# Kernel tuning notes

Hardware: AMD Instinct MI355X
Metric: run time of the kernel (lower is better)

The kernel has to match this reference:

```python
import jax, jax.numpy as jnp
import numpy as np

NUM_HEADS = 16
NUM_UNITS = 1024
NEG = -2.0**32 + 1.0
EPS = 1e-8


def setup_inputs() -> dict:
    key = jax.random.key(0)
    ks = jax.random.split(key, 8)
    B, T, C = 2, 2048, 1024
    U = NUM_UNITS
    x = jax.random.normal(ks[0], (B, T, C), dtype=jnp.float32)
    s = 1.0 / np.sqrt(C)
    Wq = jax.random.normal(ks[1], (C, U), dtype=jnp.float32) * s
    Wk = jax.random.normal(ks[2], (C, U), dtype=jnp.float32) * s
    Wv = jax.random.normal(ks[3], (C, U), dtype=jnp.float32) * s
    bq = jnp.zeros((U,), dtype=jnp.float32)
    bk = jnp.zeros((U,), dtype=jnp.float32)
    bv = jnp.zeros((U,), dtype=jnp.float32)
    gamma = jnp.ones((U,), dtype=jnp.float32)
    beta = jnp.zeros((U,), dtype=jnp.float32)
    return {"x": x, "Wq": Wq, "bq": bq, "Wk": Wk, "bk": bk,
            "Wv": Wv, "bv": bv, "gamma": gamma, "beta": beta}


def _attention(x, Wq, bq, Wk, bk, Wv, bv, gamma, beta):
    B, T, C = x.shape
    H = NUM_HEADS
    U = NUM_UNITS
    dh = U // H
    # Dense projections with relu activation (Keras Dense(activation='relu'))
    Q = jax.nn.relu(x @ Wq + bq)  # [B, T, U]
    K = jax.nn.relu(x @ Wk + bk)
    V = jax.nn.relu(x @ Wv + bv)
    # split into heads: tf.split(axis=2) + concat(axis=0) == [B, T, H, dh]
    Qh = Q.reshape(B, T, H, dh)
    Kh = K.reshape(B, T, H, dh)
    Vh = V.reshape(B, T, H, dh)
    # scaled dot-product scores: scale by sqrt(d_head) (K_ last dim after split)
    scores = jnp.einsum('bqhd,bkhd->bhqk', Qh, Kh) / np.sqrt(dh)
    # key mask: sign(|sum(keys, -1)|) over the ORIGINAL keys input (= x)
    key_mask = jnp.sign(jnp.abs(jnp.sum(x, axis=-1)))  # [B, Tk]
    scores = jnp.where(key_mask[:, None, None, :] == 0, NEG, scores)
    # causal mask (lower-triangular)
    tril = jnp.tril(jnp.ones((T, T), dtype=scores.dtype))
    scores = jnp.where(tril[None, None, :, :] == 0, NEG, scores)
    attn = jax.nn.softmax(scores, axis=-1)
    # query mask: multiply attention rows for zero queries
    query_mask = jnp.sign(jnp.abs(jnp.sum(x, axis=-1)))  # [B, Tq]
    attn = attn * query_mask[:, None, :, None]
    # dropout rate is 0 -> identity
    out = jnp.einsum('bhqk,bkhd->bqhd', attn, Vh).reshape(B, T, U)
    # residual with original queries
    out = out + x
    # layer norm over last axis (tf.nn.moments: biased variance)
    mean = jnp.mean(out, axis=-1, keepdims=True)
    var = jnp.mean((out - mean) ** 2, axis=-1, keepdims=True)
    normalized = (out - mean) / jnp.sqrt(var + EPS)
    return gamma * normalized + beta


def reference(x, Wq, bq, Wk, bk, Wv, bv, gamma, beta):
    return _attention(x, Wq, bq, Wk, bk, Wv, bv, gamma, beta)
```

## Files before the change

### kernel.cpp

```cpp
#include <hip/hip_runtime.h>
#include <math.h>

#define BB 2
#define TT 2048
#define CC 1024
#define UU 1024
#define HH 16
#define DH 64
#define BT (BB*TT)

typedef __attribute__((ext_vector_type(8))) __bf16 bf16x8;
typedef __attribute__((ext_vector_type(4))) __bf16 bf16x4;
typedef __attribute__((ext_vector_type(4))) float f32x4;

#define GLL16(g, l) __builtin_amdgcn_global_load_lds( \
    (__attribute__((address_space(1))) const void*)(g), \
    (__attribute__((address_space(3))) void*)(l), 16, 0, 0)

#define C2EXP 0.18033688011112042f
#define MBIAS 64.0f

__global__ __launch_bounds__(256) void prep_kernel(
    const float* __restrict__ x, float* __restrict__ kadd, __bf16* __restrict__ xb,
    const float* __restrict__ Wq, const float* __restrict__ Wk,
    const float* __restrict__ Wv, __bf16* __restrict__ Wt) {
    const int bx = blockIdx.x;
    const int t = threadIdx.x;
    if (bx < BT) {
        int row = bx;
        float4 v = *(const float4*)&x[(size_t)row * CC + t * 4];
        bf16x4 o;
        o[0] = (__bf16)v.x; o[1] = (__bf16)v.y; o[2] = (__bf16)v.z; o[3] = (__bf16)v.w;
        *(bf16x4*)&xb[(size_t)row * CC + t * 4] = o;
        float s = v.x + v.y + v.z + v.w;
#pragma unroll
        for (int off = 32; off; off >>= 1) s += __shfl_down(s, off, 64);
        __shared__ float red[4];
        int lane = t & 63, w = t >> 6;
        if (lane == 0) red[w] = s;
        __syncthreads();
        if (t == 0) {
            float tot = red[0] + red[1] + red[2] + red[3];
            kadd[row] = (tot == 0.f ? -1.0e30f : 0.f) - MBIAS;
        }
    } else {
        int bz = bx - BT;
        int z = bz >> 8, rem = bz & 255;
        const float* W = z == 0 ? Wq : (z == 1 ? Wk : Wv);
        __bf16* Out = Wt + (size_t)z * CC * UU;
        __shared__ float tile[64][65];
        int n0 = (rem & 15) * 64, k0 = (rem >> 4) * 64;
        int r = t >> 4, c4 = (t & 15) * 4;
#pragma unroll
        for (int i = 0; i < 4; ++i) {
            float4 v = *(const float4*)&W[(size_t)(k0 + r + i * 16) * UU + n0 + c4];
            tile[r + i * 16][c4 + 0] = v.x; tile[r + i * 16][c4 + 1] = v.y;
            tile[r + i * 16][c4 + 2] = v.z; tile[r + i * 16][c4 + 3] = v.w;
        }
        __syncthreads();
#pragma unroll
        for (int i = 0; i < 4; ++i) {
            int nr = r + i * 16;
            bf16x4 o;
            o[0] = (__bf16)tile[c4 + 0][nr]; o[1] = (__bf16)tile[c4 + 1][nr];
            o[2] = (__bf16)tile[c4 + 2][nr]; o[3] = (__bf16)tile[c4 + 3][nr];
            *(bf16x4*)&Out[(size_t)(n0 + nr) * CC + k0 + c4] = o;
        }
    }
}

__global__ __launch_bounds__(256, 4) void qkv_mfma(
    const __bf16* __restrict__ xb, const __bf16* __restrict__ Wt_all,
    const float* __restrict__ bq, const float* __restrict__ bk,
    const float* __restrict__ bv,
    __bf16* __restrict__ Qo, __bf16* __restrict__ Ko, __bf16* __restrict__ VTo) {
    const int z = blockIdx.z;
    const __bf16* Wt = Wt_all + (size_t)z * CC * UU;
    const float* bias = z == 0 ? bq : (z == 1 ? bk : bv);

    const int n0 = blockIdx.x * 128, m0 = blockIdx.y * 128;
    const int t = threadIdx.x, w = t >> 6, lane = t & 63;
    const int quad = lane >> 4, nn = lane & 15;
    const int wr = w >> 1, wc = w & 1;

    __shared__ __bf16 smem[2 * 128 * 64];
    __bf16* As = smem;
    __bf16* Bs = smem + 128 * 64;

    f32x4 acc[4][4];
#pragma unroll
    for (int i = 0; i < 4; ++i)
#pragma unroll
        for (int j = 0; j < 4; ++j) acc[i][j] = (f32x4){0.f, 0.f, 0.f, 0.f};

    for (int k0 = 0; k0 < CC; k0 += 64) {
        __syncthreads();
#pragma unroll
        for (int i = 0; i < 4; ++i) {
            int c = i * 256 + t;
            int row = c >> 3;
            int gc = ((c & 7) ^ (row & 7)) * 8;
            GLL16(&xb[(size_t)(m0 + row) * CC + k0 + gc], &As[c * 8]);
            GLL16(&Wt[(size_t)(n0 + row) * CC + k0 + gc], &Bs[c * 8]);
        }
        __syncthreads();
#pragma unroll
        for (int kk = 0; kk < 2; ++kk) {
            bf16x8 af[4], bfr[4];
#pragma unroll
            for (int i = 0; i < 4; ++i) {
                int R = wr * 64 + i * 16 + nn;
                af[i] = *(const bf16x8*)&As[R * 64 + (((kk * 4 + quad) ^ (R & 7)) * 8)];
            }
#pragma unroll
            for (int j = 0; j < 4; ++j) {
                int R = wc * 64 + j * 16 + nn;
                bfr[j] = *(const bf16x8*)&Bs[R * 64 + (((kk * 4 + quad) ^ (R & 7)) * 8)];
            }
#pragma unroll
            for (int i = 0; i < 4; ++i)
#pragma unroll
                for (int j = 0; j < 4; ++j)
                    acc[i][j] = __builtin_amdgcn_mfma_f32_16x16x32_bf16(af[i], bfr[j], acc[i][j], 0, 0, 0);
        }
    }

    __bf16* cw = &smem[w * 1024];
    float bv4[4];
#pragma unroll
    for (int j = 0; j < 4; ++j) bv4[j] = bias[n0 + wc * 64 + j * 16 + nn];

    if (z < 2) {
        __bf16* Out = z == 0 ? Qo : Ko;
#pragma unroll
        for (int i = 0; i < 4; ++i) {
            __syncthreads();
#pragma unroll
            for (int j = 0; j < 4; ++j)
#pragma unroll
                for (int r = 0; r < 4; ++r)
                    cw[(quad * 4 + r) * 64 + j * 16 + nn] =
                        (__bf16)fmaxf(acc[i][j][r] + bv4[j], 0.f);
            __syncthreads();
            int rr = lane >> 2, cc = (lane & 3) * 16;
            bf16x8 v0 = *(const bf16x8*)&cw[rr * 64 + cc];
            bf16x8 v1 = *(const bf16x8*)&cw[rr * 64 + cc + 8];
            size_t o = (size_t)(m0 + wr * 64 + i * 16 + rr) * UU + n0 + wc * 64 + cc;
            *(bf16x8*)&Out[o] = v0;
            *(bf16x8*)&Out[o + 8] = v1;
        }
    } else {
#pragma unroll
        for (int i = 0; i < 4; ++i) {
            __syncthreads();
#pragma unroll
            for (int j = 0; j < 4; ++j)
#pragma unroll
                for (int r = 0; r < 4; ++r)
                    cw[(j * 16 + nn) * 16 + quad * 4 + r] =
                        (__bf16)fmaxf(acc[i][j][r] + bv4[j], 0.f);
            __syncthreads();
            bf16x8 v0 = *(const bf16x8*)&cw[lane * 16];
            bf16x8 v1 = *(const bf16x8*)&cw[lane * 16 + 8];
            size_t o = (size_t)(n0 + wc * 64 + lane) * BT + m0 + wr * 64 + i * 16;
            *(bf16x8*)&VTo[o] = v0;
            *(bf16x8*)&VTo[o + 8] = v1;
        }
    }
}

__global__ __launch_bounds__(256, 4) void attn_mfma(
    const __bf16* __restrict__ Q, const __bf16* __restrict__ K,
    const __bf16* __restrict__ Vt, const float* __restrict__ kadd,
    __bf16* __restrict__ Ob) {
    const int bx = blockIdx.x;
    const int bh = blockIdx.y, b = bh >> 4, h = bh & 15;
    const int j = bh >> 3;
    const int xj = (j & 2) ? ((bx + 16) & 31) : bx;
    const int qt = (j & 1) ? (31 - xj) : xj;
    const int col0 = h * 64, rowbase = b * TT, q0 = qt * 64;

    const int t = threadIdx.x;
    const int w = t >> 6, lane = t & 63, quad = lane >> 4, nn = lane & 15;
    const int s7 = nn & 7;

    __shared__ __align__(16) __bf16 ks[2][64 * 64];
    __shared__ __align__(16) __bf16 vt[2][64 * 64];
    __shared__ __align__(16) __bf16 ps[64 * 64];

    const int c0 = t, c1 = 256 + t;
    const int r0 = c0 >> 3, g0 = ((c0 & 7) ^ (r0 & 7)) * 8;
    const int r1 = c1 >> 3, g1 = ((c1 & 7) ^ (r1 & 7)) * 8;

    GLL16(&Q[(size_t)(rowbase + q0 + r0) * UU + col0 + g0], &ps[c0 * 8]);
    GLL16(&Q[(size_t)(rowbase + q0 + r1) * UU + col0 + g1], &ps[c1 * 8]);
    GLL16(&K[(size_t)(rowbase + r0) * UU + col0 + g0], &ks[0][c0 * 8]);
    GLL16(&K[(size_t)(rowbase + r1) * UU + col0 + g1], &ks[0][c1 * 8]);
    GLL16(&Vt[(size_t)(col0 + r0) * BT + rowbase + g0], &vt[0][c0 * 8]);
    GLL16(&Vt[(size_t)(col0 + r1) * BT + rowbase + g1], &vt[0][c1 * 8]);
    __syncthreads();

    const int prow = 16 * w + nn;
    bf16x8 bq0 = *(const bf16x8*)&ps[prow * 64 + ((quad ^ (prow & 7)) * 8)];
    bf16x8 bq1 = *(const bf16x8*)&ps[prow * 64 + (((4 + quad) ^ (prow & 7)) * 8)];

    float lp = 0.f;
    f32x4 oc[4];
#pragma unroll
    for (int dt = 0; dt < 4; ++dt) oc[dt] = (f32x4){0.f, 0.f, 0.f, 0.f};
    const int qg = q0 + 16 * w + nn;

    for (int kt = 0; kt <= qt; ++kt) {
        const int cur = kt & 1;
        const int k0 = kt * 64;
        f32x4 ka[4];
#pragma unroll
        for (int ct = 0; ct < 4; ++ct)
            ka[ct] = *(const f32x4*)&kadd[rowbase + k0 + ct * 16 + quad * 4];
        if (kt < qt) {
            const int kn = k0 + 64;
            GLL16(&K[(size_t)(rowbase + kn + r0) * UU + col0 + g0], &ks[cur ^ 1][c0 * 8]);
            GLL16(&K[(size_t)(rowbase + kn + r1) * UU + col0 + g1], &ks[cur ^ 1][c1 * 8]);
            GLL16(&Vt[(size_t)(col0 + r0) * BT + rowbase + kn + g0], &vt[cur ^ 1][c0 * 8]);
            GLL16(&Vt[(size_t)(col0 + r1) * BT + rowbase + kn + g1], &vt[cur ^ 1][c1 * 8]);
        }

        const bool diag = (kt == qt);
        const __bf16* ksc = ks[cur];
        const __bf16* vtc = vt[cur];

#pragma unroll
        for (int ct = 0; ct < 4; ++ct) {
            int krow = ct * 16 + nn;
            bf16x8 a0 = *(const bf16x8*)&ksc[krow * 64 + ((quad ^ s7) * 8)];
            bf16x8 a1 = *(const bf16x8*)&ksc[krow * 64 + (((4 + quad) ^ s7) * 8)];
            f32x4 sc = (f32x4){0.f, 0.f, 0.f, 0.f};
            sc = __builtin_amdgcn_mfma_f32_16x16x32_bf16(a0, bq0, sc, 0, 0, 0);
            sc = __builtin_amdgcn_mfma_f32_16x16x32_bf16(a1, bq1, sc, 0, 0, 0);
            bf16x4 pw;
#pragma unroll
            for (int r = 0; r < 4; ++r) {
                int key = k0 + ct * 16 + quad * 4 + r;
                float arg = fmaf(sc[r], C2EXP, ka[ct][r]);
                if (diag && key > qg) arg = -1.0e30f;
                float p = exp2f(arg);
                lp += p;
                pw[r] = (__bf16)p;
            }
            int chunk = ct * 2 + (quad >> 1);
            *(bf16x4*)&ps[prow * 64 + ((chunk ^ (prow & 7)) * 8) + (quad & 1) * 4] = pw;
        }
        bf16x8 bp0 = *(const bf16x8*)&ps[prow * 64 + ((quad ^ (prow & 7)) * 8)];
        bf16x8 bp1 = *(const bf16x8*)&ps[prow * 64 + (((4 + quad) ^ (prow & 7)) * 8)];
#pragma unroll
        for (int dt = 0; dt < 4; ++dt) {
            int vrow = dt * 16 + nn;
            bf16x8 a0 = *(const bf16x8*)&vtc[vrow * 64 + ((quad ^ s7) * 8)];
            bf16x8 a1 = *(const bf16x8*)&vtc[vrow * 64 + (((4 + quad) ^ s7) * 8)];
            oc[dt] = __builtin_amdgcn_mfma_f32_16x16x32_bf16(a0, bp0, oc[dt], 0, 0, 0);
            oc[dt] = __builtin_amdgcn_mfma_f32_16x16x32_bf16(a1, bp1, oc[dt], 0, 0, 0);
        }
        __syncthreads();
    }

    float l = lp;
    l += __shfl_xor(l, 16, 64);
    l += __shfl_xor(l, 32, 64);
    int grow = rowbase + qg;
    float qsel = (kadd[grow] < -1.0e29f) ? 0.f : 1.f;
    float mult = qsel / fmaxf(l, 1e-37f);
#pragma unroll
    for (int dt = 0; dt < 4; ++dt) {
        bf16x4 ov;
        ov[0] = (__bf16)(oc[dt][0] * mult); ov[1] = (__bf16)(oc[dt][1] * mult);
        ov[2] = (__bf16)(oc[dt][2] * mult); ov[3] = (__bf16)(oc[dt][3] * mult);
        *(bf16x4*)&Ob[(size_t)grow * UU + col0 + dt * 16 + quad * 4] = ov;
    }
}

__global__ __launch_bounds__(256) void ln_kernel(
    const __bf16* __restrict__ Ob, const float* __restrict__ x,
    const float* __restrict__ gamma, const float* __restrict__ beta,
    float* __restrict__ out) {
    int row = blockIdx.x;
    size_t base = (size_t)row * UU;
    int t = threadIdx.x;
    bf16x4 ov = *(const bf16x4*)&Ob[base + t * 4];
    float4 xv = *(const float4*)&x[base + t * 4];
    float v0 = (float)ov[0] + xv.x, v1 = (float)ov[1] + xv.y;
    float v2 = (float)ov[2] + xv.z, v3 = (float)ov[3] + xv.w;
    float s1 = v0 + v1 + v2 + v3;
    float s2 = v0 * v0 + v1 * v1 + v2 * v2 + v3 * v3;
#pragma unroll
    for (int off = 32; off; off >>= 1) {
        s1 += __shfl_down(s1, off, 64);
        s2 += __shfl_down(s2, off, 64);
    }
    __shared__ float r1[4], r2[4];
    int lane = t & 63, w = t >> 6;
    if (lane == 0) { r1[w] = s1; r2[w] = s2; }
    __syncthreads();
    s1 = r1[0] + r1[1] + r1[2] + r1[3];
    s2 = r2[0] + r2[1] + r2[2] + r2[3];
    float mean = s1 * (1.0f / 1024.0f);
    float var = s2 * (1.0f / 1024.0f) - mean * mean;
    float rstd = rsqrtf(var + 1e-8f);
    float4 g = *(const float4*)&gamma[t * 4];
    float4 be = *(const float4*)&beta[t * 4];
    float4 ores;
    ores.x = g.x * (v0 - mean) * rstd + be.x;
    ores.y = g.y * (v1 - mean) * rstd + be.y;
    ores.z = g.z * (v2 - mean) * rstd + be.z;
    ores.w = g.w * (v3 - mean) * rstd + be.w;
    *(float4*)&out[base + t * 4] = ores;
}

extern "C" void kernel_launch(void* const* d_in, const int* in_sizes, int n_in,
                              void* d_out, int out_size, void* d_ws, size_t ws_size,
                              hipStream_t stream) {
    const float* x     = (const float*)d_in[0];
    const float* Wq    = (const float*)d_in[1];
    const float* bq    = (const float*)d_in[2];
    const float* Wk    = (const float*)d_in[3];
    const float* bk    = (const float*)d_in[4];
    const float* Wv    = (const float*)d_in[5];
    const float* bv    = (const float*)d_in[6];
    const float* gamma = (const float*)d_in[7];
    const float* beta  = (const float*)d_in[8];
    float* out = (float*)d_out;

    char* wsb = (char*)d_ws;
    const size_t MB = 1024ull * 1024;
    __bf16* xb = (__bf16*)(wsb);
    __bf16* Wt = (__bf16*)(wsb + 8 * MB);
    __bf16* Ob = (__bf16*)(wsb);
    __bf16* Qb = (__bf16*)(wsb + 16 * MB);
    __bf16* Kb = (__bf16*)(wsb + 24 * MB);
    __bf16* Vt = (__bf16*)(wsb + 32 * MB);
    float* kadd = (float*)(wsb + 40 * MB);

    prep_kernel<<<dim3(BT + 768), dim3(256), 0, stream>>>(x, kadd, xb, Wq, Wk, Wv, Wt);
    qkv_mfma<<<dim3(UU / 128, BT / 128, 3), dim3(256), 0, stream>>>(
        xb, Wt, bq, bk, bv, Qb, Kb, Vt);
    attn_mfma<<<dim3(32, BB * HH), dim3(256), 0, stream>>>(Qb, Kb, Vt, kadd, Ob);
    ln_kernel<<<dim3(BT), dim3(256), 0, stream>>>(Ob, x, gamma, beta, out);
}
```

Measured before the change: 173.8 us.

## Enlarge attention query tile to 128 rows with 512-thread blocks sharing K/V tiles

The attention kernel now handles 128 query rows per block with 8 waves instead of 64 rows with 4 waves, so each K/V tile loaded into shared memory is reused by twice as many query rows. This halves K/V global traffic per query and halves the block count. Waves covering the first 64 rows skip the last key tile, and the diagonal mask is computed per half. The costs are fewer blocks in flight, a simpler load-balancing remap, more shared memory per block, and idle waves on the final tile.

```diff
diff --git a/kernel.cpp b/kernel.cpp
--- a/kernel.cpp
+++ b/kernel.cpp
@@ -169,16 +169,15 @@
     }
 }
 
-__global__ __launch_bounds__(256, 4) void attn_mfma(
+__global__ __launch_bounds__(512, 4) void attn_mfma(
     const __bf16* __restrict__ Q, const __bf16* __restrict__ K,
     const __bf16* __restrict__ Vt, const float* __restrict__ kadd,
     __bf16* __restrict__ Ob) {
     const int bx = blockIdx.x;
     const int bh = blockIdx.y, b = bh >> 4, h = bh & 15;
     const int j = bh >> 3;
-    const int xj = (j & 2) ? ((bx + 16) & 31) : bx;
-    const int qt = (j & 1) ? (31 - xj) : xj;
-    const int col0 = h * 64, rowbase = b * TT, q0 = qt * 64;
+    const int qt = (j & 2) ? (15 - bx) : bx;
+    const int col0 = h * 64, rowbase = b * TT, q0 = qt * 128;
 
     const int t = threadIdx.x;
     const int w = t >> 6, lane = t & 63, quad = lane >> 4, nn = lane & 15;
@@ -186,79 +185,80 @@
 
     __shared__ __align__(16) __bf16 ks[2][64 * 64];
     __shared__ __align__(16) __bf16 vt[2][64 * 64];
-    __shared__ __align__(16) __bf16 ps[64 * 64];
-
-    const int c0 = t, c1 = 256 + t;
-    const int r0 = c0 >> 3, g0 = ((c0 & 7) ^ (r0 & 7)) * 8;
-    const int r1 = c1 >> 3, g1 = ((c1 & 7) ^ (r1 & 7)) * 8;
-
-    GLL16(&Q[(size_t)(rowbase + q0 + r0) * UU + col0 + g0], &ps[c0 * 8]);
+    __shared__ __align__(16) __bf16 ps[128 * 64];
+
+    const int r0 = t >> 3, g0 = ((t & 7) ^ (r0 & 7)) * 8;
+    const int c1 = 512 + t, r1 = c1 >> 3, g1 = ((c1 & 7) ^ (r1 & 7)) * 8;
+
+    GLL16(&Q[(size_t)(rowbase + q0 + r0) * UU + col0 + g0], &ps[t * 8]);
     GLL16(&Q[(size_t)(rowbase + q0 + r1) * UU + col0 + g1], &ps[c1 * 8]);
-    GLL16(&K[(size_t)(rowbase + r0) * UU + col0 + g0], &ks[0][c0 * 8]);
-    GLL16(&K[(size_t)(rowbase + r1) * UU + col0 + g1], &ks[0][c1 * 8]);
-    GLL16(&Vt[(size_t)(col0 + r0) * BT + rowbase + g0], &vt[0][c0 * 8]);
-    GLL16(&Vt[(size_t)(col0 + r1) * BT + rowbase + g1], &vt[0][c1 * 8]);
+    GLL16(&K[(size_t)(rowbase + r0) * UU + col0 + g0], &ks[0][t * 8]);
+    GLL16(&Vt[(size_t)(col0 + r0) * BT + rowbase + g0], &vt[0][t * 8]);
     __syncthreads();
 
-    const int prow = 16 * w + nn;
-    bf16x8 bq0 = *(const bf16x8*)&ps[prow * 64 + ((quad ^ (prow & 7)) * 8)];
-    bf16x8 bq1 = *(const bf16x8*)&ps[prow * 64 + (((4 + quad) ^ (prow & 7)) * 8)];
+    const int prow = (w & 3) * 16 + nn + ((w >> 2) << 6);
+    const int p7 = prow & 7;
+    bf16x8 bq0 = *(const bf16x8*)&ps[prow * 64 + ((quad ^ p7) * 8)];
+    bf16x8 bq1 = *(const bf16x8*)&ps[prow * 64 + (((4 + quad) ^ p7) * 8)];
 
     float lp = 0.f;
     f32x4 oc[4];
 #pragma unroll
     for (int dt = 0; dt < 4; ++dt) oc[dt] = (f32x4){0.f, 0.f, 0.f, 0.f};
-    const int qg = q0 + 16 * w + nn;
-
-    for (int kt = 0; kt <= qt; ++kt) {
+    const int lr = prow & 63;
+    const int qg = q0 + prow;
+    const int kend = 2 * qt + 1;
+
+    for (int kt = 0; kt <= kend; ++kt) {
         const int cur = kt & 1;
         const int k0 = kt * 64;
         f32x4 ka[4];
 #pragma unroll
         for (int ct = 0; ct < 4; ++ct)
             ka[ct] = *(const f32x4*)&kadd[rowbase + k0 + ct * 16 + quad * 4];
-        if (kt < qt) {
+        if (kt < kend) {
             const int kn = k0 + 64;
-            GLL16(&K[(size_t)(rowbase + kn + r0) * UU + col0 + g0], &ks[cur ^ 1][c0 * 8]);
-            GLL16(&K[(size_t)(rowbase + kn + r1) * UU + col0 + g1], &ks[cur ^ 1][c1 * 8]);
-            GLL16(&Vt[(size_t)(col0 + r0) * BT + rowbase + kn + g0], &vt[cur ^ 1][c0 * 8]);
-            GLL16(&Vt[(size_t)(col0 + r1) * BT + rowbase + kn + g1], &vt[cur ^ 1][c1 * 8]);
-        }
-
-        const bool diag = (kt == qt);
-        const __bf16* ksc = ks[cur];
-        const __bf16* vtc = vt[cur];
-
-#pragma unroll
-        for (int ct = 0; ct < 4; ++ct) {
-            int krow = ct * 16 + nn;
-            bf16x8 a0 = *(const bf16x8*)&ksc[krow * 64 + ((quad ^ s7) * 8)];
-            bf16x8 a1 = *(const bf16x8*)&ksc[krow * 64 + (((4 + quad) ^ s7) * 8)];
-            f32x4 sc = (f32x4){0.f, 0.f, 0.f, 0.f};
-            sc = __builtin_amdgcn_mfma_f32_16x16x32_bf16(a0, bq0, sc, 0, 0, 0);
-            sc = __builtin_amdgcn_mfma_f32_16x16x32_bf16(a1, bq1, sc, 0, 0, 0);
-            bf16x4 pw;
-#pragma unroll
-            for (int r = 0; r < 4; ++r) {
-                int key = k0 + ct * 16 + quad * 4 + r;
-                float arg = fmaf(sc[r], C2EXP, ka[ct][r]);
-                if (diag && key > qg) arg = -1.0e30f;
-                float p = exp2f(arg);
-                lp += p;
-                pw[r] = (__bf16)p;
+            GLL16(&K[(size_t)(rowbase + kn + r0) * UU + col0 + g0], &ks[cur ^ 1][t * 8]);
+            GLL16(&Vt[(size_t)(col0 + r0) * BT + rowbase + kn + g0], &vt[cur ^ 1][t * 8]);
+        }
+
+        const bool skip = (w < 4) && (kt == kend);
+        if (!skip) {
+            const bool diag = (kt == kend - 1 + (w >> 2));
+            const __bf16* ksc = ks[cur];
+            const __bf16* vtc = vt[cur];
+
+#pragma unroll
+            for (int ct = 0; ct < 4; ++ct) {
+                int krow = ct * 16 + nn;
+                bf16x8 a0 = *(const bf16x8*)&ksc[krow * 64 + ((quad ^ s7) * 8)];
+                bf16x8 a1 = *(const bf16x8*)&ksc[krow * 64 + (((4 + quad) ^ s7) * 8)];
+                f32x4 sc = (f32x4){0.f, 0.f, 0.f, 0.f};
+                sc = __builtin_amdgcn_mfma_f32_16x16x32_bf16(a0, bq0, sc, 0, 0, 0);
+                sc = __builtin_amdgcn_mfma_f32_16x16x32_bf16(a1, bq1, sc, 0, 0, 0);
+                bf16x4 pw;
+#pragma unroll
+                for (int r = 0; r < 4; ++r) {
+                    int kl = ct * 16 + quad * 4 + r;
+                    float arg = fmaf(sc[r], C2EXP, ka[ct][r]);
+                    if (diag && kl > lr) arg = -1.0e30f;
+                    float p = exp2f(arg);
+                    lp += p;
+                    pw[r] = (__bf16)p;
+                }
+                int chunk = ct * 2 + (quad >> 1);
+                *(bf16x4*)&ps[prow * 64 + ((chunk ^ p7) * 8) + (quad & 1) * 4] = pw;
             }
-            int chunk = ct * 2 + (quad >> 1);
-            *(bf16x4*)&ps[prow * 64 + ((chunk ^ (prow & 7)) * 8) + (quad & 1) * 4] = pw;
-        }
-        bf16x8 bp0 = *(const bf16x8*)&ps[prow * 64 + ((quad ^ (prow & 7)) * 8)];
-        bf16x8 bp1 = *(const bf16x8*)&ps[prow * 64 + (((4 + quad) ^ (prow & 7)) * 8)];
-#pragma unroll
-        for (int dt = 0; dt < 4; ++dt) {
-            int vrow = dt * 16 + nn;
-            bf16x8 a0 = *(const bf16x8*)&vtc[vrow * 64 + ((quad ^ s7) * 8)];
-            bf16x8 a1 = *(const bf16x8*)&vtc[vrow * 64 + (((4 + quad) ^ s7) * 8)];
-            oc[dt] = __builtin_amdgcn_mfma_f32_16x16x32_bf16(a0, bp0, oc[dt], 0, 0, 0);
-            oc[dt] = __builtin_amdgcn_mfma_f32_16x16x32_bf16(a1, bp1, oc[dt], 0, 0, 0);
+            bf16x8 bp0 = *(const bf16x8*)&ps[prow * 64 + ((quad ^ p7) * 8)];
+            bf16x8 bp1 = *(const bf16x8*)&ps[prow * 64 + (((4 + quad) ^ p7) * 8)];
+#pragma unroll
+            for (int dt = 0; dt < 4; ++dt) {
+                int vrow = dt * 16 + nn;
+                bf16x8 a0 = *(const bf16x8*)&vtc[vrow * 64 + ((quad ^ s7) * 8)];
+                bf16x8 a1 = *(const bf16x8*)&vtc[vrow * 64 + (((4 + quad) ^ s7) * 8)];
+                oc[dt] = __builtin_amdgcn_mfma_f32_16x16x32_bf16(a0, bp0, oc[dt], 0, 0, 0);
+                oc[dt] = __builtin_amdgcn_mfma_f32_16x16x32_bf16(a1, bp1, oc[dt], 0, 0, 0);
+            }
         }
         __syncthreads();
     }
@@ -342,6 +342,6 @@
     prep_kernel<<<dim3(BT + 768), dim3(256), 0, stream>>>(x, kadd, xb, Wq, Wk, Wv, Wt);
     qkv_mfma<<<dim3(UU / 128, BT / 128, 3), dim3(256), 0, stream>>>(
         xb, Wt, bq, bk, bv, Qb, Kb, Vt);
-    attn_mfma<<<dim3(32, BB * HH), dim3(256), 0, stream>>>(Qb, Kb, Vt, kadd, Ob);
+    attn_mfma<<<dim3(16, BB * HH), dim3(512), 0, stream>>>(Qb, Kb, Vt, kadd, Ob);
     ln_kernel<<<dim3(BT), dim3(256), 0, stream>>>(Ob, x, gamma, beta, out);
 }
```

Result: slower. 181.7 us (+4.5%).

## Triple-buffer K tiles with explicit vmcnt waits in causal attention kernel

Applied to the files above, without the earlier changes.

Restructures the attention main loop so K is prefetched two tiles ahead in a triple buffer and V one tile ahead, synchronising with fine-grained s_waitcnt vmcnt plus s_barrier instead of a full __syncthreads. Q fragments now load straight from global memory into registers rather than staging through LDS, kadd values are prefetched one iteration ahead, and the diagonal tile is peeled so the main loop carries no mask check. The intent is to hide global load latency behind the MFMA work. The extra LDS buffer lowers the occupancy hint from 4 to 3 blocks per CU. Inline asm wait counts and reads from fixed ring offsets make correctness depend on the exact ordering of the loads.

```diff
diff --git a/kernel.cpp b/kernel.cpp
--- a/kernel.cpp
+++ b/kernel.cpp
@@ -169,7 +169,7 @@
     }
 }
 
-__global__ __launch_bounds__(256, 4) void attn_mfma(
+__global__ __launch_bounds__(256, 3) void attn_mfma(
     const __bf16* __restrict__ Q, const __bf16* __restrict__ K,
     const __bf16* __restrict__ Vt, const float* __restrict__ kadd,
     __bf16* __restrict__ Ob) {
@@ -184,84 +184,113 @@
     const int w = t >> 6, lane = t & 63, quad = lane >> 4, nn = lane & 15;
     const int s7 = nn & 7;
 
-    __shared__ __align__(16) __bf16 ks[2][64 * 64];
+    __shared__ __align__(16) __bf16 ks[3][64 * 64];
     __shared__ __align__(16) __bf16 vt[2][64 * 64];
     __shared__ __align__(16) __bf16 ps[64 * 64];
 
-    const int c0 = t, c1 = 256 + t;
+    const int c0 = t;
     const int r0 = c0 >> 3, g0 = ((c0 & 7) ^ (r0 & 7)) * 8;
-    const int r1 = c1 >> 3, g1 = ((c1 & 7) ^ (r1 & 7)) * 8;
-
-    GLL16(&Q[(size_t)(rowbase + q0 + r0) * UU + col0 + g0], &ps[c0 * 8]);
-    GLL16(&Q[(size_t)(rowbase + q0 + r1) * UU + col0 + g1], &ps[c1 * 8]);
-    GLL16(&K[(size_t)(rowbase + r0) * UU + col0 + g0], &ks[0][c0 * 8]);
-    GLL16(&K[(size_t)(rowbase + r1) * UU + col0 + g1], &ks[0][c1 * 8]);
-    GLL16(&Vt[(size_t)(col0 + r0) * BT + rowbase + g0], &vt[0][c0 * 8]);
-    GLL16(&Vt[(size_t)(col0 + r1) * BT + rowbase + g1], &vt[0][c1 * 8]);
-    __syncthreads();
-
     const int prow = 16 * w + nn;
-    bf16x8 bq0 = *(const bf16x8*)&ps[prow * 64 + ((quad ^ (prow & 7)) * 8)];
-    bf16x8 bq1 = *(const bf16x8*)&ps[prow * 64 + (((4 + quad) ^ (prow & 7)) * 8)];
+    const int qg = q0 + prow;
+
+    const __bf16* kp0 = &K[(size_t)(rowbase + r0) * UU + col0 + g0];
+    const __bf16* kp1 = kp0 + 32 * (size_t)UU;
+    const __bf16* vp0 = &Vt[(size_t)(col0 + r0) * BT + rowbase + g0];
+    const __bf16* vp1 = vp0 + 32 * (size_t)BT;
+    const float* kap = &kadd[rowbase + quad * 4];
+
+    f32x4 ka[4];
+#pragma unroll
+    for (int ct = 0; ct < 4; ++ct) ka[ct] = *(const f32x4*)&kap[ct * 16];
+    kap += 64;
+    const __bf16* qrow = &Q[(size_t)(rowbase + qg) * UU + col0];
+    bf16x8 bq0 = *(const bf16x8*)&qrow[quad * 8];
+    bf16x8 bq1 = *(const bf16x8*)&qrow[32 + quad * 8];
+    __builtin_amdgcn_sched_barrier(0);
+    GLL16(kp0, &ks[0][c0 * 8]);
+    GLL16(kp1, &ks[0][c0 * 8 + 2048]);
+    GLL16(vp0, &vt[0][c0 * 8]);
+    GLL16(vp1, &vt[0][c0 * 8 + 2048]);
+    kp0 += 64 * (size_t)UU; kp1 += 64 * (size_t)UU;
+    vp0 += 64; vp1 += 64;
+    __builtin_amdgcn_sched_barrier(0);
+    GLL16(kp0, &ks[0][4096 + c0 * 8]);
+    GLL16(kp1, &ks[0][4096 + c0 * 8 + 2048]);
+    kp0 += 64 * (size_t)UU; kp1 += 64 * (size_t)UU;
+    __builtin_amdgcn_sched_barrier(0);
+    asm volatile("s_waitcnt vmcnt(2)" ::: "memory");
+    __builtin_amdgcn_s_barrier();
 
     float lp = 0.f;
     f32x4 oc[4];
 #pragma unroll
     for (int dt = 0; dt < 4; ++dt) oc[dt] = (f32x4){0.f, 0.f, 0.f, 0.f};
-    const int qg = q0 + 16 * w + nn;
-
-    for (int kt = 0; kt <= qt; ++kt) {
-        const int cur = kt & 1;
-        const int k0 = kt * 64;
-        f32x4 ka[4];
-#pragma unroll
-        for (int ct = 0; ct < 4; ++ct)
-            ka[ct] = *(const f32x4*)&kadd[rowbase + k0 + ct * 16 + quad * 4];
-        if (kt < qt) {
-            const int kn = k0 + 64;
-            GLL16(&K[(size_t)(rowbase + kn + r0) * UU + col0 + g0], &ks[cur ^ 1][c0 * 8]);
-            GLL16(&K[(size_t)(rowbase + kn + r1) * UU + col0 + g1], &ks[cur ^ 1][c1 * 8]);
-            GLL16(&Vt[(size_t)(col0 + r0) * BT + rowbase + kn + g0], &vt[cur ^ 1][c0 * 8]);
-            GLL16(&Vt[(size_t)(col0 + r1) * BT + rowbase + kn + g1], &vt[cur ^ 1][c1 * 8]);
-        }
-
-        const bool diag = (kt == qt);
-        const __bf16* ksc = ks[cur];
-        const __bf16* vtc = vt[cur];
-
-#pragma unroll
-        for (int ct = 0; ct < 4; ++ct) {
-            int krow = ct * 16 + nn;
-            bf16x8 a0 = *(const bf16x8*)&ksc[krow * 64 + ((quad ^ s7) * 8)];
-            bf16x8 a1 = *(const bf16x8*)&ksc[krow * 64 + (((4 + quad) ^ s7) * 8)];
-            f32x4 sc = (f32x4){0.f, 0.f, 0.f, 0.f};
-            sc = __builtin_amdgcn_mfma_f32_16x16x32_bf16(a0, bq0, sc, 0, 0, 0);
-            sc = __builtin_amdgcn_mfma_f32_16x16x32_bf16(a1, bq1, sc, 0, 0, 0);
-            bf16x4 pw;
-#pragma unroll
-            for (int r = 0; r < 4; ++r) {
-                int key = k0 + ct * 16 + quad * 4 + r;
-                float arg = fmaf(sc[r], C2EXP, ka[ct][r]);
-                if (diag && key > qg) arg = -1.0e30f;
-                float p = exp2f(arg);
-                lp += p;
-                pw[r] = (__bf16)p;
-            }
-            int chunk = ct * 2 + (quad >> 1);
-            *(bf16x4*)&ps[prow * 64 + ((chunk ^ (prow & 7)) * 8) + (quad & 1) * 4] = pw;
-        }
-        bf16x8 bp0 = *(const bf16x8*)&ps[prow * 64 + ((quad ^ (prow & 7)) * 8)];
-        bf16x8 bp1 = *(const bf16x8*)&ps[prow * 64 + (((4 + quad) ^ (prow & 7)) * 8)];
-#pragma unroll
-        for (int dt = 0; dt < 4; ++dt) {
-            int vrow = dt * 16 + nn;
-            bf16x8 a0 = *(const bf16x8*)&vtc[vrow * 64 + ((quad ^ s7) * 8)];
-            bf16x8 a1 = *(const bf16x8*)&vtc[vrow * 64 + (((4 + quad) ^ s7) * 8)];
-            oc[dt] = __builtin_amdgcn_mfma_f32_16x16x32_bf16(a0, bp0, oc[dt], 0, 0, 0);
-            oc[dt] = __builtin_amdgcn_mfma_f32_16x16x32_bf16(a1, bp1, oc[dt], 0, 0, 0);
-        }
-        __syncthreads();
-    }
+
+#define ATTN_CORE(KOFF, VOFF, DIAG)                                            \
+  {                                                                            \
+    const __bf16* ksc = &ks[0][0] + (KOFF);                                    \
+    const __bf16* vtc = &vt[0][0] + (VOFF);                                    \
+    _Pragma("unroll")                                                          \
+    for (int ct = 0; ct < 4; ++ct) {                                           \
+      int krow = ct * 16 + nn;                                                 \
+      bf16x8 a0 = *(const bf16x8*)&ksc[krow * 64 + ((quad ^ s7) * 8)];         \
+      bf16x8 a1 = *(const bf16x8*)&ksc[krow * 64 + (((4 + quad) ^ s7) * 8)];   \
+      f32x4 sc = (f32x4){0.f, 0.f, 0.f, 0.f};                                  \
+      sc = __builtin_amdgcn_mfma_f32_16x16x32_bf16(a0, bq0, sc, 0, 0, 0);      \
+      sc = __builtin_amdgcn_mfma_f32_16x16x32_bf16(a1, bq1, sc, 0, 0, 0);      \
+      bf16x4 pw;                                                               \
+      _Pragma("unroll")                                                        \
+      for (int r = 0; r < 4; ++r) {                                            \
+        float arg = fmaf(sc[r], C2EXP, ka[ct][r]);                             \
+        if (DIAG) {                                                            \
+          int kl = ct * 16 + quad * 4 + r;                                     \
+          if (kl > prow) arg = -1.0e30f;                                       \
+        }                                                                      \
+        float p = __builtin_amdgcn_exp2f(arg);                                 \
+        lp += p;                                                               \
+        pw[r] = (__bf16)p;                                                     \
+      }                                                                        \
+      int chunk = ct * 2 + (quad >> 1);                                        \
+      *(bf16x4*)&ps[prow * 64 + ((chunk ^ s7) * 8) + (quad & 1) * 4] = pw;     \
+    }                                                                          \
+    bf16x8 bp0 = *(const bf16x8*)&ps[prow * 64 + ((quad ^ s7) * 8)];           \
+    bf16x8 bp1 = *(const bf16x8*)&ps[prow * 64 + (((4 + quad) ^ s7) * 8)];     \
+    _Pragma("unroll")                                                          \
+    for (int dt = 0; dt < 4; ++dt) {                                           \
+      int vrow = dt * 16 + nn;                                                 \
+      bf16x8 a0 = *(const bf16x8*)&vtc[vrow * 64 + ((quad ^ s7) * 8)];         \
+      bf16x8 a1 = *(const bf16x8*)&vtc[vrow * 64 + (((4 + quad) ^ s7) * 8)];   \
+      oc[dt] = __builtin_amdgcn_mfma_f32_16x16x32_bf16(a0, bp0, oc[dt], 0, 0, 0); \
+      oc[dt] = __builtin_amdgcn_mfma_f32_16x16x32_bf16(a1, bp1, oc[dt], 0, 0, 0); \
+    }                                                                          \
+  }
+
+    int kro = 0, kwo = 2 * 4096, vo = 0;
+    for (int kt = 0; kt < qt; ++kt) {
+        f32x4 kan[4];
+#pragma unroll
+        for (int ct = 0; ct < 4; ++ct) kan[ct] = *(const f32x4*)&kap[ct * 16];
+        kap += 64;
+        __builtin_amdgcn_sched_barrier(0);
+        GLL16(vp0, &vt[0][(vo ^ 4096) + c0 * 8]);
+        GLL16(vp1, &vt[0][(vo ^ 4096) + c0 * 8 + 2048]);
+        vp0 += 64; vp1 += 64;
+        __builtin_amdgcn_sched_barrier(0);
+        GLL16(kp0, &ks[0][kwo + c0 * 8]);
+        GLL16(kp1, &ks[0][kwo + c0 * 8 + 2048]);
+        kp0 += 64 * (size_t)UU; kp1 += 64 * (size_t)UU;
+        __builtin_amdgcn_sched_barrier(0);
+        ATTN_CORE(kro, vo, false)
+#pragma unroll
+        for (int ct = 0; ct < 4; ++ct) ka[ct] = kan[ct];
+        kro = kro == 8192 ? 0 : kro + 4096;
+        kwo = kwo == 8192 ? 0 : kwo + 4096;
+        vo ^= 4096;
+        asm volatile("s_waitcnt vmcnt(2)" ::: "memory");
+        __builtin_amdgcn_s_barrier();
+    }
+    ATTN_CORE(kro, vo, true)
+#undef ATTN_CORE
 
     float l = lp;
     l += __shfl_xor(l, 16, 64);
```

New measurement: 171.1 us. Within noise of the previous version (-1.5%).
